# Performance work log

Measured on AMD Instinct MI355X. Metric: run time of the kernel, lower is better.

Reference implementation:

```python
import jax, jax.numpy as jnp
import numpy as np

N = 50000
E = 800000
IN_DIM = 256
HID = 128
HEADS = 2
OUT_DIM = 256
NEG_SLOPE = 0.2  # DGL GATConv default


def gat_layer(x, W, a_l, a_r, b, src, dst, num_nodes):
    """One DGL-style GATConv layer (eval mode, no dropout).
    x: [N, Fin]; W: [Fin, heads*d]; a_l, a_r: [heads, d]; b: [heads, d].
    Returns [N, heads, d].
    """
    heads, d = a_l.shape
    z = (x @ W).reshape(num_nodes, heads, d)              # [N, heads, d]
    el = jnp.einsum('nhd,hd->nh', z, a_l)                 # [N, heads]
    er = jnp.einsum('nhd,hd->nh', z, a_r)                 # [N, heads]
    e = el[src] + er[dst]                                 # [E, heads]
    e = jnp.where(e > 0, e, NEG_SLOPE * e)                # LeakyReLU
    # segment softmax over incoming edges of each dst node
    m = jax.ops.segment_max(e, dst, num_segments=num_nodes)   # [N, heads]
    ex = jnp.exp(e - m[dst])                               # [E, heads]
    s = jax.ops.segment_sum(ex, dst, num_segments=num_nodes)  # [N, heads]
    alpha = ex / s[dst]                                    # [E, heads]
    # weighted scatter-add aggregation
    msg = z[src] * alpha[:, :, None]                       # [E, heads, d]
    out = jax.ops.segment_sum(msg, dst, num_segments=num_nodes)  # [N, heads, d]
    return out + b[None, :, :]


def setup_inputs() -> dict:
    key = jax.random.key(0)
    ks = jax.random.split(key, 12)
    sc1 = 1.0 / np.sqrt(IN_DIM)
    sc2 = 1.0 / np.sqrt(HEADS * HID)
    return {
        'node_feats': jax.random.normal(ks[0], (N, IN_DIM), dtype=jnp.float32),
        'src': jax.random.randint(ks[1], (E,), 0, N, dtype=jnp.int32),
        'dst': jax.random.randint(ks[2], (E,), 0, N, dtype=jnp.int32),
        'W1': jax.random.normal(ks[3], (IN_DIM, HEADS * HID), dtype=jnp.float32) * sc1,
        'al1': jax.random.normal(ks[4], (HEADS, HID), dtype=jnp.float32) * sc1,
        'ar1': jax.random.normal(ks[5], (HEADS, HID), dtype=jnp.float32) * sc1,
        'b1': jnp.zeros((HEADS, HID), dtype=jnp.float32),
        'W2': jax.random.normal(ks[6], (HEADS * HID, OUT_DIM), dtype=jnp.float32) * sc2,
        'al2': jax.random.normal(ks[7], (1, OUT_DIM), dtype=jnp.float32) * sc2,
        'ar2': jax.random.normal(ks[8], (1, OUT_DIM), dtype=jnp.float32) * sc2,
        'b2': jnp.zeros((1, OUT_DIM), dtype=jnp.float32),
    }


def reference(node_feats, src, dst, W1, al1, ar1, b1, W2, al2, ar2, b2):
    h = gat_layer(node_feats, W1, al1, ar1, b1, src, dst, N)   # [N, heads, HID]
    h = jax.nn.relu(h.reshape(N, HEADS * HID))                 # flatten(1) + relu
    out = gat_layer(h, W2, al2, ar2, b2, src, dst, N)          # [N, 1, OUT_DIM]
    return out[:, 0, :]                                        # squeeze(1)
```

## Files before the change

kernel.cpp:

```cpp
#include <hip/hip_runtime.h>
#include <hip/hip_fp16.h>
#include <math.h>


typedef _Float16 half8 __attribute__((ext_vector_type(8)));
typedef float floatx4 __attribute__((ext_vector_type(4)));

__device__ __forceinline__ float rl_f(float x, int i) {
  return __int_as_float(__builtin_amdgcn_readlane(__float_as_int(x), i));
}
__device__ __forceinline__ unsigned pk2(float a, float b) {
  return (unsigned)__half_as_ushort(__float2half_rn(a)) |
         ((unsigned)__half_as_ushort(__float2half_rn(b)) << 16);
}

__device__ __forceinline__ void fma_row(float4& acc, uint2 zv, float e) {
  union { uint2 u; __half h[4]; } w;
  w.u = zv;
  acc.x = fmaf(__half2float(w.h[0]), e, acc.x);
  acc.y = fmaf(__half2float(w.h[1]), e, acc.y);
  acc.z = fmaf(__half2float(w.h[2]), e, acc.z);
  acc.w = fmaf(__half2float(w.h[3]), e, acc.w);
}

__global__ __launch_bounds__(256) void prep(const float* __restrict__ W1,
                                            const float* __restrict__ W2,
                                            unsigned short* __restrict__ w1t,
                                            unsigned short* __restrict__ w2t,
                                            const float4* __restrict__ x,
                                            uint2* __restrict__ xh, int n4cvt,
                                            float4* __restrict__ zp, int zn4, int NZ) {
  const int b = blockIdx.x, t = threadIdx.x;
  if (b < 512) {
    const float* W = (b < 256) ? W1 : W2;
    unsigned short* Wt = (b < 256) ? w1t : w2t;
    const int k = b & 255;
    Wt[t * 256 + k] = __half_as_ushort(__float2half_rn(W[k * 256 + t]));
  } else if (b < 512 + NZ) {
    const int i = (b - 512) * 256 + t;
    if (i < zn4) zp[i] = make_float4(0.f, 0.f, 0.f, 0.f);
  } else {
    const int i = (b - 512 - NZ) * 256 + t;
    if (i < n4cvt) {
      float4 v = x[i];
      uint2 o;
      o.x = pk2(v.x, v.y);
      o.y = pk2(v.z, v.w);
      xh[i] = o;
    }
  }
}

__global__ __launch_bounds__(256) void hist_rank(const int* __restrict__ dst,
                                                 int* __restrict__ counts,
                                                 int* __restrict__ erank, int E) {
  int i = blockIdx.x * 256 + threadIdx.x;
  if (i < E) erank[i] = atomicAdd(&counts[dst[i]], 1);
}

__global__ __launch_bounds__(256) void scatter_pos(const int* __restrict__ src,
                                                   const int* __restrict__ dst,
                                                   const int* __restrict__ offs,
                                                   const int* __restrict__ erank,
                                                   int* __restrict__ esrc, int E) {
  int i = blockIdx.x * 256 + threadIdx.x;
  if (i < E) esrc[offs[dst[i]] + erank[i]] = src[i];
}

__global__ __launch_bounds__(256) void scan_block(const int* __restrict__ counts,
                                                  int* __restrict__ offsets,
                                                  int* __restrict__ bsum, int Nn) {
  __shared__ int sm[256];
  int t = threadIdx.x;
  int i = blockIdx.x * 256 + t;
  int v = (i < Nn) ? counts[i] : 0;
  sm[t] = v;
  __syncthreads();
  for (int off = 1; off < 256; off <<= 1) {
    int x = (t >= off) ? sm[t - off] : 0;
    __syncthreads();
    sm[t] += x;
    __syncthreads();
  }
  if (i < Nn) offsets[i] = sm[t] - v;
  if (t == 255) bsum[blockIdx.x] = sm[255];
}

__global__ __launch_bounds__(256) void scan_add2(int* __restrict__ offsets,
                                                 const int* __restrict__ bsum,
                                                 int Nn, int NB) {
  __shared__ int sm[256];
  const int t = threadIdx.x, b = blockIdx.x;
  int v = (t < NB && t < b) ? bsum[t] : 0;
  sm[t] = v;
  __syncthreads();
  for (int off = 1; off < 256; off <<= 1) {
    int x = (t >= off) ? sm[t - off] : 0;
    __syncthreads();
    sm[t] += x;
    __syncthreads();
  }
  const int bofs = sm[255];
  const int i = b * 256 + t;
  if (i < Nn) offsets[i] += bofs;
}


__device__ __forceinline__ void gemm_load_a(half8* af, const unsigned short* __restrict__ A,
                                            int row, int kg) {
  const unsigned short* ap = A + (size_t)row * 256 + kg * 8;
#pragma unroll
  for (int kb = 0; kb < 8; kb++) af[kb] = *(const half8*)(ap + kb * 32);
}

template <int HS>
__device__ __forceinline__ void gemm_compute_store(const half8 (&bf)[8][4], const half8* af,
                                                   int m0, int lane, int ln, int kg, int wv,
                                                   const float* __restrict__ al,
                                                   const float* __restrict__ ar,
                                                   float* __restrict__ el,
                                                   float* __restrict__ er,
                                                   unsigned short* __restrict__ C, int M) {
  floatx4 acc[4];
#pragma unroll
  for (int t = 0; t < 4; t++) acc[t] = (floatx4)0.f;
#pragma unroll
  for (int kb = 0; kb < 8; kb++)
#pragma unroll
    for (int t = 0; t < 4; t++)
      acc[t] = __builtin_amdgcn_mfma_f32_16x16x32_f16(bf[kb][t], af[kb], acc[t], 0, 0, 0);

  const int cb = wv * 64 + kg * 4;
  float pl = 0.f, pr = 0.f;
#pragma unroll
  for (int t = 0; t < 4; t++) {
    float4 av = *(const float4*)(al + cb + t * 16);
    float4 rv = *(const float4*)(ar + cb + t * 16);
    pl += acc[t].x * av.x + acc[t].y * av.y + acc[t].z * av.z + acc[t].w * av.w;
    pr += acc[t].x * rv.x + acc[t].y * rv.y + acc[t].z * rv.z + acc[t].w * rv.w;
  }
  pl += __shfl_xor(pl, 16); pl += __shfl_xor(pl, 32);
  pr += __shfl_xor(pr, 16); pr += __shfl_xor(pr, 32);

  const int row = m0 + ln;
  if (row < M) {
    if (lane < 16) {
      const int idx = HS ? (row * 2 + (wv >> 1)) : row;
      atomicAdd(&el[idx], pl);
      atomicAdd(&er[idx], pr);
    }
    unsigned short* cp = C + (size_t)row * 256 + wv * 64 + kg * 4;
#pragma unroll
    for (int t = 0; t < 4; t++) {
      uint2 o;
      o.x = pk2(acc[t].x, acc[t].y);
      o.y = pk2(acc[t].z, acc[t].w);
      *(uint2*)(cp + t * 16) = o;
    }
  }
}

template <int HS>
__global__ __launch_bounds__(256, 2) void gemm_mfma(const unsigned short* __restrict__ A,
                                                    const unsigned short* __restrict__ Wt,
                                                    unsigned short* __restrict__ C,
                                                    const float* __restrict__ al,
                                                    const float* __restrict__ ar,
                                                    float* __restrict__ el,
                                                    float* __restrict__ er, int M) {
  const int tid = threadIdx.x;
  const int wv = tid >> 6, lane = tid & 63;
  const int ln = lane & 15, kg = lane >> 4;

  half8 bf[8][4];
#pragma unroll
  for (int kb = 0; kb < 8; kb++)
#pragma unroll
    for (int t = 0; t < 4; t++)
      bf[kb][t] = *(const half8*)(Wt + (size_t)((4 * wv + t) * 16 + ln) * 256 +
                                  kb * 32 + kg * 8);

  const int nchunk = (M + 15) >> 4;
  const int stride = gridDim.x;
  int c0 = blockIdx.x;
  if (c0 >= nchunk) return;

  half8 af0[8], af1[8];
  gemm_load_a(af0, A, min(c0 * 16 + ln, M - 1), kg);
  int c1 = c0 + stride;

  for (;;) {
    if (c1 < nchunk) gemm_load_a(af1, A, min(c1 * 16 + ln, M - 1), kg);
    gemm_compute_store<HS>(bf, af0, c0 << 4, lane, ln, kg, wv, al, ar, el, er, C, M);
    if (c1 >= nchunk) break;
    const int c2 = c1 + stride;
    if (c2 < nchunk) gemm_load_a(af0, A, min(c2 * 16 + ln, M - 1), kg);
    gemm_compute_store<HS>(bf, af1, c1 << 4, lane, ln, kg, wv, al, ar, el, er, C, M);
    if (c2 >= nchunk) break;
    c0 = c2;
    c1 = c2 + stride;
  }
}

template <int HS, int RELU, int OUTH>
__global__ __launch_bounds__(256) void node_aggregate(const unsigned short* __restrict__ z,
                                                      const float* __restrict__ el,
                                                      const float* __restrict__ er,
                                                      const int* __restrict__ esrc,
                                                      const int* __restrict__ offsets,
                                                      const int* __restrict__ counts,
                                                      const float* __restrict__ bias,
                                                      void* __restrict__ out,
                                                      int n0, int cnt_nodes) {
  int wid = (blockIdx.x * 256 + threadIdx.x) >> 6;
  int lane = threadIdx.x & 63;
  if (wid >= cnt_nodes) return;
  const int n = n0 + wid;
  const int beg = offsets[n];
  const int deg = counts[n];
  float ern0, ern1 = 0.f;
  if (HS) {
    float2 e = ((const float2*)er)[n];
    ern0 = e.x; ern1 = e.y;
  } else {
    ern0 = er[n];
  }
  const int head = HS ? (lane >> 5) : 0;

  float s0 = 0.f, s1 = 0.f;
  float4 acc = make_float4(0.f, 0.f, 0.f, 0.f);
  const uint2* zp = (const uint2*)z;

  for (int base = 0; base < deg; base += 64) {
    const int cnt = min(64, deg - base);
    int sn = 0;
    float myex0 = 0.f, myex1 = 0.f;
    if (lane < cnt) {
      sn = esrc[beg + base + lane];
      if (HS) {
        float2 elv = ((const float2*)el)[sn];
        float v0 = elv.x + ern0; v0 = (v0 > 0.f) ? v0 : 0.2f * v0;
        float v1 = elv.y + ern1; v1 = (v1 > 0.f) ? v1 : 0.2f * v1;
        myex0 = __expf(v0);
        myex1 = __expf(v1);
      } else {
        float v0 = el[sn] + ern0; v0 = (v0 > 0.f) ? v0 : 0.2f * v0;
        myex0 = __expf(v0);
      }
      s0 += myex0;
      s1 += myex1;
    }

    int i = 0;
    for (; i + 8 <= cnt; i += 8) {
      int s_[8];
      float e_[8];
      uint2 zv[8];
#pragma unroll
      for (int j = 0; j < 8; j++) {
        s_[j] = __builtin_amdgcn_readlane(sn, i + j);
        float e0 = rl_f(myex0, i + j);
        if (HS) {
          float e1 = rl_f(myex1, i + j);
          e_[j] = head ? e1 : e0;
        } else {
          e_[j] = e0;
        }
      }
#pragma unroll
      for (int j = 0; j < 8; j++) zv[j] = zp[((size_t)s_[j] << 6) + lane];
#pragma unroll
      for (int j = 0; j < 8; j++) fma_row(acc, zv[j], e_[j]);
    }
    for (; i < cnt; i++) {
      int si = __builtin_amdgcn_readlane(sn, i);
      float e = rl_f(myex0, i);
      if (HS) {
        float e1 = rl_f(myex1, i);
        if (head) e = e1;
      }
      uint2 zv = zp[((size_t)si << 6) + lane];
      fma_row(acc, zv, e);
    }
  }

#pragma unroll
  for (int o = 32; o > 0; o >>= 1) {
    s0 += __shfl_xor(s0, o);
    if (HS) s1 += __shfl_xor(s1, o);
  }
  const float s = (HS && head) ? s1 : s0;
  float4 bb = ((const float4*)bias)[lane];
  float4 v;
  if (deg > 0) {
    float inv = 1.f / s;
    v = make_float4(acc.x * inv + bb.x, acc.y * inv + bb.y,
                    acc.z * inv + bb.z, acc.w * inv + bb.w);
  } else {
    v = bb;
  }
  if (RELU) {
    v.x = fmaxf(v.x, 0.f); v.y = fmaxf(v.y, 0.f);
    v.z = fmaxf(v.z, 0.f); v.w = fmaxf(v.w, 0.f);
  }
  if (OUTH) {
    uint2 o;
    o.x = pk2(v.x, v.y);
    o.y = pk2(v.z, v.w);
    ((uint2*)out)[((size_t)n << 6) + lane] = o;
  } else {
    ((float4*)out)[((size_t)n << 6) + lane] = v;
  }
}

extern "C" void kernel_launch(void* const* d_in, const int* in_sizes, int n_in,
                              void* d_out, int out_size, void* d_ws, size_t ws_size,
                              hipStream_t stream) {
  const float* x   = (const float*)d_in[0];
  const int*   src = (const int*)d_in[1];
  const int*   dst = (const int*)d_in[2];
  const float* W1  = (const float*)d_in[3];
  const float* al1 = (const float*)d_in[4];
  const float* ar1 = (const float*)d_in[5];
  const float* b1  = (const float*)d_in[6];
  const float* W2  = (const float*)d_in[7];
  const float* al2 = (const float*)d_in[8];
  const float* ar2 = (const float*)d_in[9];
  const float* b2  = (const float*)d_in[10];
  float* out = (float*)d_out;
  (void)n_in; (void)out_size; (void)ws_size;

  const int Nn = in_sizes[0] / 256;
  const int Ee = in_sizes[1];
  const int F = 256;
  const int NB = (Nn + 255) / 256;

  unsigned short* z   = (unsigned short*)d_ws;
  unsigned short* xh  = z + (size_t)Nn * F;
  unsigned short* w1t = xh + (size_t)Nn * F;
  unsigned short* w2t = w1t + 65536;
  int*   esrc   = (int*)(w2t + 65536);
  int*   counts = esrc + Ee;
  int*   offs   = counts + Nn;
  int*   cursor = offs + Nn;
  int*   bsum   = cursor + Nn;
  int*   bofs   = bsum + 256;
  float* el1p   = (float*)(bofs + 256);
  float* er1p   = el1p + (size_t)Nn * 2;
  float* el2p   = er1p + (size_t)Nn * 2;
  float* er2p   = el2p + Nn;
  int*   erank  = (int*)z;

  dim3 blk(256);

  const int zn4 = (9 * Nn + 512) / 4;
  const int NZ = (zn4 + 255) / 256;
  const int n4cvt = Nn * 64;
  const int NC = (n4cvt + 255) / 256;
  prep<<<512 + NZ + NC, blk, 0, stream>>>(W1, W2, w1t, w2t, (const float4*)x,
                                          (uint2*)xh, n4cvt, (float4*)counts, zn4, NZ);

  const int EB = (Ee + 255) / 256;
  hist_rank<<<EB, blk, 0, stream>>>(dst, counts, erank, Ee);
  scan_block<<<NB, blk, 0, stream>>>(counts, offs, bsum, Nn);
  scan_add2<<<NB, blk, 0, stream>>>(offs, bsum, Nn, NB);
  scatter_pos<<<EB, blk, 0, stream>>>(src, dst, offs, erank, esrc, Ee);

  const int gemm_grid = 512;

  gemm_mfma<1><<<gemm_grid, blk, 0, stream>>>(xh, w1t, z, al1, ar1, el1p, er1p, Nn);
  node_aggregate<1, 1, 1><<<(Nn + 3) / 4, blk, 0, stream>>>(z, el1p, er1p, esrc, offs,
                                                            counts, b1, xh, 0, Nn);

  gemm_mfma<0><<<gemm_grid, blk, 0, stream>>>(xh, w2t, z, al2, ar2, el2p, er2p, Nn);
  node_aggregate<0, 0, 0><<<(Nn + 3) / 4, blk, 0, stream>>>(z, el2p, er2p, esrc, offs,
                                                            counts, b2, out, 0, Nn);
}
```

Measured before the change: 346.0 us.

## Fuse edge scatter into first GEMM and replace el/er atomics with LDS reduction

```diff
diff --git a/kernel.cpp b/kernel.cpp
--- a/kernel.cpp
+++ b/kernel.cpp
@@ -58,15 +58,6 @@
   if (i < E) erank[i] = atomicAdd(&counts[dst[i]], 1);
 }
 
-__global__ __launch_bounds__(256) void scatter_pos(const int* __restrict__ src,
-                                                   const int* __restrict__ dst,
-                                                   const int* __restrict__ offs,
-                                                   const int* __restrict__ erank,
-                                                   int* __restrict__ esrc, int E) {
-  int i = blockIdx.x * 256 + threadIdx.x;
-  if (i < E) esrc[offs[dst[i]] + erank[i]] = src[i];
-}
-
 __global__ __launch_bounds__(256) void scan_block(const int* __restrict__ counts,
                                                   int* __restrict__ offsets,
                                                   int* __restrict__ bsum, int Nn) {
@@ -115,12 +106,14 @@
 
 template <int HS>
 __device__ __forceinline__ void gemm_compute_store(const half8 (&bf)[8][4], const half8* af,
-                                                   int m0, int lane, int ln, int kg, int wv,
+                                                   int m0, int tid, int lane, int ln, int kg,
+                                                   int wv, int par,
                                                    const float* __restrict__ al,
                                                    const float* __restrict__ ar,
                                                    float* __restrict__ el,
                                                    float* __restrict__ er,
-                                                   unsigned short* __restrict__ C, int M) {
+                                                   unsigned short* __restrict__ C, int M,
+                                                   float* __restrict__ lred) {
   floatx4 acc[4];
 #pragma unroll
   for (int t = 0; t < 4; t++) acc[t] = (floatx4)0.f;
@@ -142,13 +135,36 @@
   pl += __shfl_xor(pl, 16); pl += __shfl_xor(pl, 32);
   pr += __shfl_xor(pr, 16); pr += __shfl_xor(pr, 32);
 
+  if (lane < 16) {
+    lred[((par * 2 + 0) * 4 + wv) * 16 + lane] = pl;
+    lred[((par * 2 + 1) * 4 + wv) * 16 + lane] = pr;
+  }
+  __syncthreads();
+
+  if (HS) {
+    if (tid < 64) {
+      const int sel = tid >> 5, rh = tid & 31, r = rh >> 1, h = rh & 1;
+      if (m0 + r < M) {
+        float v = lred[((par * 2 + sel) * 4 + 2 * h) * 16 + r] +
+                  lred[((par * 2 + sel) * 4 + 2 * h + 1) * 16 + r];
+        (sel ? er : el)[(m0 + r) * 2 + h] = v;
+      }
+    }
+  } else {
+    if (tid < 32) {
+      const int sel = tid >> 4, r = tid & 15;
+      if (m0 + r < M) {
+        float v = lred[((par * 2 + sel) * 4 + 0) * 16 + r] +
+                  lred[((par * 2 + sel) * 4 + 1) * 16 + r] +
+                  lred[((par * 2 + sel) * 4 + 2) * 16 + r] +
+                  lred[((par * 2 + sel) * 4 + 3) * 16 + r];
+        (sel ? er : el)[m0 + r] = v;
+      }
+    }
+  }
+
   const int row = m0 + ln;
   if (row < M) {
-    if (lane < 16) {
-      const int idx = HS ? (row * 2 + (wv >> 1)) : row;
-      atomicAdd(&el[idx], pl);
-      atomicAdd(&er[idx], pr);
-    }
     unsigned short* cp = C + (size_t)row * 256 + wv * 64 + kg * 4;
 #pragma unroll
     for (int t = 0; t < 4; t++) {
@@ -160,14 +176,20 @@
   }
 }
 
-template <int HS>
+template <int HS, int SCAT>
 __global__ __launch_bounds__(256, 2) void gemm_mfma(const unsigned short* __restrict__ A,
                                                     const unsigned short* __restrict__ Wt,
                                                     unsigned short* __restrict__ C,
                                                     const float* __restrict__ al,
                                                     const float* __restrict__ ar,
                                                     float* __restrict__ el,
-                                                    float* __restrict__ er, int M) {
+                                                    float* __restrict__ er, int M,
+                                                    const int* __restrict__ src,
+                                                    const int* __restrict__ dst,
+                                                    const int* __restrict__ offs,
+                                                    const int* __restrict__ erank,
+                                                    int* __restrict__ esrc, int E) {
+  __shared__ float lred[2 * 2 * 4 * 16];
   const int tid = threadIdx.x;
   const int wv = tid >> 6, lane = tid & 63;
   const int ln = lane & 15, kg = lane >> 4;
@@ -183,22 +205,33 @@
   const int nchunk = (M + 15) >> 4;
   const int stride = gridDim.x;
   int c0 = blockIdx.x;
-  if (c0 >= nchunk) return;
-
-  half8 af0[8], af1[8];
-  gemm_load_a(af0, A, min(c0 * 16 + ln, M - 1), kg);
-  int c1 = c0 + stride;
-
-  for (;;) {
-    if (c1 < nchunk) gemm_load_a(af1, A, min(c1 * 16 + ln, M - 1), kg);
-    gemm_compute_store<HS>(bf, af0, c0 << 4, lane, ln, kg, wv, al, ar, el, er, C, M);
-    if (c1 >= nchunk) break;
-    const int c2 = c1 + stride;
-    if (c2 < nchunk) gemm_load_a(af0, A, min(c2 * 16 + ln, M - 1), kg);
-    gemm_compute_store<HS>(bf, af1, c1 << 4, lane, ln, kg, wv, al, ar, el, er, C, M);
-    if (c2 >= nchunk) break;
-    c0 = c2;
-    c1 = c2 + stride;
+
+  if (c0 < nchunk) {
+    half8 af0[8], af1[8];
+    gemm_load_a(af0, A, min(c0 * 16 + ln, M - 1), kg);
+    int c1 = c0 + stride;
+
+    for (;;) {
+      if (c1 < nchunk) gemm_load_a(af1, A, min(c1 * 16 + ln, M - 1), kg);
+      gemm_compute_store<HS>(bf, af0, c0 << 4, tid, lane, ln, kg, wv, 0,
+                             al, ar, el, er, C, M, lred);
+      if (c1 >= nchunk) break;
+      const int c2 = c1 + stride;
+      if (c2 < nchunk) gemm_load_a(af0, A, min(c2 * 16 + ln, M - 1), kg);
+      gemm_compute_store<HS>(bf, af1, c1 << 4, tid, lane, ln, kg, wv, 1,
+                             al, ar, el, er, C, M, lred);
+      if (c2 >= nchunk) break;
+      c0 = c2;
+      c1 = c2 + stride;
+    }
+  }
+
+  if (SCAT) {
+    const int per = (E + (int)gridDim.x - 1) / (int)gridDim.x;
+    const int b0 = blockIdx.x * per;
+    const int b1 = min(E, b0 + per);
+    for (int i = b0 + tid; i < b1; i += 256)
+      esrc[offs[dst[i]] + erank[i]] = src[i];
   }
 }
 
@@ -349,7 +382,7 @@
   float* er1p   = el1p + (size_t)Nn * 2;
   float* el2p   = er1p + (size_t)Nn * 2;
   float* er2p   = el2p + Nn;
-  int*   erank  = (int*)z;
+  int*   erank  = (int*)d_out;
 
   dim3 blk(256);
 
@@ -364,15 +397,17 @@
   hist_rank<<<EB, blk, 0, stream>>>(dst, counts, erank, Ee);
   scan_block<<<NB, blk, 0, stream>>>(counts, offs, bsum, Nn);
   scan_add2<<<NB, blk, 0, stream>>>(offs, bsum, Nn, NB);
-  scatter_pos<<<EB, blk, 0, stream>>>(src, dst, offs, erank, esrc, Ee);
 
   const int gemm_grid = 512;
 
-  gemm_mfma<1><<<gemm_grid, blk, 0, stream>>>(xh, w1t, z, al1, ar1, el1p, er1p, Nn);
+  gemm_mfma<1, 1><<<gemm_grid, blk, 0, stream>>>(xh, w1t, z, al1, ar1, el1p, er1p, Nn,
+                                                 src, dst, offs, erank, esrc, Ee);
   node_aggregate<1, 1, 1><<<(Nn + 3) / 4, blk, 0, stream>>>(z, el1p, er1p, esrc, offs,
                                                             counts, b1, xh, 0, Nn);
 
-  gemm_mfma<0><<<gemm_grid, blk, 0, stream>>>(xh, w2t, z, al2, ar2, el2p, er2p, Nn);
+  gemm_mfma<0, 0><<<gemm_grid, blk, 0, stream>>>(xh, w2t, z, al2, ar2, el2p, er2p, Nn,
+                                                 nullptr, nullptr, nullptr, nullptr,
+                                                 nullptr, 0);
   node_aggregate<0, 0, 0><<<(Nn + 3) / 4, blk, 0, stream>>>(z, el2p, er2p, esrc, offs,
                                                             counts, b2, out, 0, Nn);
 }
```

Result: slower. 366.6 us (+5.9%).
